# Kernel optimization log

Measured on AMD Instinct MI355X. Metric: run time of the kernel, lower is better.

Reference implementation:

```python
import jax, jax.numpy as jnp
import numpy as np
from jax import lax

B, CIN, H, W = 2, 512, 64, 64
CD = CIN // 2            # down_dim = 256
CQ = CD // 8             # q/k channels = 32
EPS = 1e-5               # BatchNorm eps


def _conv3(x, w, b):
    # 3x3 conv, stride 1, padding 1 (init padding=1), NCHW/OIHW
    y = lax.conv_general_dilated(x, w, (1, 1), [(1, 1), (1, 1)],
                                 dimension_numbers=('NCHW', 'OIHW', 'NCHW'))
    return y + b[None, :, None, None]


def _bn(x, g, b, m, v):
    scale = g / jnp.sqrt(v + EPS)
    return x * scale[None, :, None, None] + (b - m * scale)[None, :, None, None]


def _prelu(x, a):
    return jnp.where(x > 0, x, a * x)


def _p1(x, w, b):
    # 1x1 conv as channel matmul
    return jnp.einsum('bchw,oc->bohw', x, w) + b[None, :, None, None]


def setup_inputs() -> dict:
    key = jax.random.key(0)
    it = iter(jax.random.split(key, 64))
    def nrm(shape, s=0.05):
        return jax.random.normal(next(it), shape, jnp.float32) * s
    inp = {
        'input_rgb': jax.random.normal(next(it), (B, CIN, H, W), jnp.float32),
        'input_dsm': jax.random.normal(next(it), (B, CIN, H, W), jnp.float32),
    }
    for m in ('rgb', 'dsm'):
        inp['conv_w_' + m] = nrm((CD, CIN, 3, 3))
        inp['conv_b_' + m] = nrm((CD,))
        inp['bn_g_' + m] = 1.0 + nrm((CD,))
        inp['bn_b_' + m] = nrm((CD,))
        inp['bn_m_' + m] = nrm((CD,))
        inp['bn_v_' + m] = jax.random.uniform(next(it), (CD,), jnp.float32, 0.5, 1.5)
        inp['prelu_' + m] = jnp.float32(0.25)
        inp['q_w_' + m] = nrm((CQ, CD)); inp['q_b_' + m] = nrm((CQ,))
        inp['k_w_' + m] = nrm((CQ, CD)); inp['k_b_' + m] = nrm((CQ,))
        inp['v_w_' + m] = nrm((CD, CD)); inp['v_b_' + m] = nrm((CD,))
        inp['up_w_' + m] = nrm((CIN, CD)); inp['up_b_' + m] = nrm((CIN,))
        inp['gamma_' + m] = jnp.float32(0.1)  # learned residual gate (zero-init in torch)
    return inp


def reference(input_rgb, input_dsm,
              conv_w_rgb, conv_b_rgb, bn_g_rgb, bn_b_rgb, bn_m_rgb, bn_v_rgb, prelu_rgb,
              q_w_rgb, q_b_rgb, k_w_rgb, k_b_rgb, v_w_rgb, v_b_rgb, up_w_rgb, up_b_rgb, gamma_rgb,
              conv_w_dsm, conv_b_dsm, bn_g_dsm, bn_b_dsm, bn_m_dsm, bn_v_dsm, prelu_dsm,
              q_w_dsm, q_b_dsm, k_w_dsm, k_b_dsm, v_w_dsm, v_b_dsm, up_w_dsm, up_b_dsm, gamma_dsm):
    conv_rgb = _prelu(_bn(_conv3(input_rgb, conv_w_rgb, conv_b_rgb),
                          bn_g_rgb, bn_b_rgb, bn_m_rgb, bn_v_rgb), prelu_rgb)
    conv_dsm = _prelu(_bn(_conv3(input_dsm, conv_w_dsm, conv_b_dsm),
                          bn_g_dsm, bn_b_dsm, bn_m_dsm, bn_v_dsm), prelu_dsm)
    b, c, h, w = conv_rgb.shape
    n = h * w
    q_rgb = _p1(conv_rgb, q_w_rgb, q_b_rgb).reshape(b, CQ, n)
    k_rgb = _p1(conv_rgb, k_w_rgb, k_b_rgb).reshape(b, CQ, n)
    v_rgb = _p1(conv_rgb, v_w_rgb, v_b_rgb).reshape(b, c, n)
    q_dsm = _p1(conv_dsm, q_w_dsm, q_b_dsm).reshape(b, CQ, n)
    k_dsm = _p1(conv_dsm, k_w_dsm, k_b_dsm).reshape(b, CQ, n)
    v_dsm = _p1(conv_dsm, v_w_dsm, v_b_dsm).reshape(b, c, n)
    # cross-modal unscaled attention: dsm queries attend over rgb keys
    attn_rgb = jax.nn.softmax(jnp.einsum('bqn,bqm->bnm', q_dsm, k_rgb), axis=-1)  # [b,n,n]
    o_rgb = jnp.einsum('bcj,bij->bci', v_rgb, attn_rgb).reshape(b, c, h, w)
    o_rgb = gamma_rgb * o_rgb + conv_rgb
    attn_dsm = jax.nn.softmax(jnp.einsum('bqn,bqm->bnm', q_rgb, k_dsm), axis=-1)
    o_dsm = jnp.einsum('bcj,bij->bci', v_dsm, attn_dsm).reshape(b, c, h, w)
    o_dsm = gamma_dsm * o_dsm + conv_dsm
    out_rgb = _p1(o_rgb, up_w_rgb, up_b_rgb) + input_rgb
    out_dsm = _p1(o_dsm, up_w_dsm, up_b_dsm) + input_dsm
    return (out_rgb, out_dsm)
```

## Files before the change

kernel.cpp:

```cpp
#include <hip/hip_runtime.h>
#include <hip/hip_bf16.h>
#include <stdint.h>


constexpr int CINCH = 512;
constexpr int NPIX  = 4096;

typedef __bf16 bf16x8 __attribute__((ext_vector_type(8)));
typedef __bf16 bf16x4 __attribute__((ext_vector_type(4)));
typedef float  f32x4  __attribute__((ext_vector_type(4)));

__device__ __forceinline__ __bf16 f2b(float f) {
    __hip_bfloat16 h = __float2bfloat16(f);
    return *reinterpret_cast<__bf16*>(&h);
}

__device__ __forceinline__ void load_lds16(const void* g, void* l) {
    __builtin_amdgcn_global_load_lds(
        (const __attribute__((address_space(1))) unsigned int*)(uintptr_t)g,
        (__attribute__((address_space(3))) unsigned int*)(uintptr_t)l,
        16, 0, 0);
}

__global__ __launch_bounds__(256)
void prep_w(const float* __restrict__ w_r, const float* __restrict__ w_d,
            const float* __restrict__ cb_r, const float* __restrict__ bg_r,
            const float* __restrict__ bb_r, const float* __restrict__ bm_r,
            const float* __restrict__ bv_r,
            const float* __restrict__ cb_d, const float* __restrict__ bg_d,
            const float* __restrict__ bb_d, const float* __restrict__ bm_d,
            const float* __restrict__ bv_d,
            __bf16* __restrict__ Wt, float* __restrict__ scA,
            float* __restrict__ shB, __bf16* __restrict__ zrow)
{
    const int t = threadIdx.x;
    const int blk = blockIdx.x;
    if (blk < 2304) {
        int gid = blk * 1024 + t * 4;
        int mod = gid >= 1179648;
        int o2  = gid - mod * 1179648;
        int tap = o2 >> 17;
        int r   = o2 & 131071;
        int oc  = r >> 9;
        int ic  = r & 511;
        const float* wsrc = mod ? w_d : w_r;
        long base = ((long)(oc * 512 + ic)) * 9 + tap;
        bf16x4 v;
        v.x = f2b(wsrc[base]);
        v.y = f2b(wsrc[base + 9]);
        v.z = f2b(wsrc[base + 18]);
        v.w = f2b(wsrc[base + 27]);
        *(bf16x4*)&Wt[gid] = v;
    } else if (blk == 2304) {
        unsigned short* z = (unsigned short*)zrow;
        z[t] = 0; z[t + 256] = 0;
    } else {
        int mod = blk - 2305;
        const float* cb = mod ? cb_d : cb_r;
        const float* bg = mod ? bg_d : bg_r;
        const float* bb = mod ? bb_d : bb_r;
        const float* bm = mod ? bm_d : bm_r;
        const float* bv = mod ? bv_d : bv_r;
        int oc = t;
        float sc = bg[oc] * rsqrtf(bv[oc] + 1e-5f);
        scA[mod * 256 + oc] = sc;
        shB[mod * 256 + oc] = (cb[oc] - bm[oc]) * sc + bb[oc];
    }
}

__global__ __launch_bounds__(256)
void prep_gw(const float* __restrict__ qw_r, const float* __restrict__ qw_d,
             const float* __restrict__ kw_r, const float* __restrict__ kw_d,
             const float* __restrict__ vw_r, const float* __restrict__ vw_d,
             const float* __restrict__ uw_r, const float* __restrict__ uw_d,
             __bf16* __restrict__ Wq, __bf16* __restrict__ Wk,
             __bf16* __restrict__ Wv, __bf16* __restrict__ Wu)
{
    int gid = blockIdx.x * 1024 + threadIdx.x * 4;
    __bf16* dst;
    float4 f = make_float4(0.f, 0.f, 0.f, 0.f);
    if (gid < 65536) {
        int mod = gid >> 15, e = gid & 32767;
        dst = Wq + gid;
        if (e < 8192) f = *(const float4*)((mod ? qw_d : qw_r) + e);
    } else if (gid < 131072) {
        int g = gid - 65536;
        int mod = g >> 15, e = g & 32767;
        dst = Wk + g;
        if (e < 8192) f = *(const float4*)((mod ? kw_d : kw_r) + e);
    } else if (gid < 262144) {
        int g = gid - 131072;
        int mod = g >> 16, e = g & 65535;
        dst = Wv + g;
        f = *(const float4*)((mod ? vw_d : vw_r) + e);
    } else {
        int g = gid - 262144;
        int mod = g >> 17, e = g & 131071;
        dst = Wu + g;
        f = *(const float4*)((mod ? uw_d : uw_r) + e);
    }
    bf16x4 o; o.x = f2b(f.x); o.y = f2b(f.y); o.z = f2b(f.z); o.w = f2b(f.w);
    *(bf16x4*)dst = o;
}

__global__ __launch_bounds__(256)
void xpose(const float* __restrict__ inr, const float* __restrict__ ind,
           __bf16* __restrict__ Xp)
{
    __shared__ float tile[32][33];
    const int t = threadIdx.x;
    const int p0 = blockIdx.x * 32;
    const int ic0 = blockIdx.y * 32;
    const int mb = blockIdx.z;
    const int mod = mb >> 1, b = mb & 1;
    const float* src = (mod ? ind : inr) + (long)b * CINCH * NPIX;

    int i = t >> 3, j4 = (t & 7) * 4;
    float4 v = *(const float4*)&src[(long)(ic0 + i) * NPIX + p0 + j4];
    tile[i][j4 + 0] = v.x; tile[i][j4 + 1] = v.y;
    tile[i][j4 + 2] = v.z; tile[i][j4 + 3] = v.w;
    __syncthreads();
    int j = t >> 3, i4 = (t & 7) * 4;
    bf16x4 o;
    o.x = f2b(tile[i4 + 0][j]);
    o.y = f2b(tile[i4 + 1][j]);
    o.z = f2b(tile[i4 + 2][j]);
    o.w = f2b(tile[i4 + 3][j]);
    *(bf16x4*)&Xp[((long)mb * NPIX + p0 + j) * 512 + ic0 + i4] = o;
}

__global__ __launch_bounds__(256)
void t256(const float* __restrict__ src, __bf16* __restrict__ dst)
{
    __shared__ float tile[32][33];
    const int t = threadIdx.x;
    const int p0 = blockIdx.x * 32;
    const int c0 = blockIdx.y * 32;
    const int mb = blockIdx.z;
    const float* s = src + (long)mb * 256 * NPIX;
    __bf16* d = dst + (long)mb * NPIX * 256;

    int i = t >> 3, j4 = (t & 7) * 4;
    float4 v = *(const float4*)&s[(long)(c0 + i) * NPIX + p0 + j4];
    tile[i][j4 + 0] = v.x; tile[i][j4 + 1] = v.y;
    tile[i][j4 + 2] = v.z; tile[i][j4 + 3] = v.w;
    __syncthreads();
    int j = t >> 3, i4 = (t & 7) * 4;
    bf16x4 o;
    o.x = f2b(tile[i4 + 0][j]); o.y = f2b(tile[i4 + 1][j]);
    o.z = f2b(tile[i4 + 2][j]); o.w = f2b(tile[i4 + 3][j]);
    *(bf16x4*)&d[((long)(p0 + j)) * 256 + c0 + i4] = o;
}

__global__ __launch_bounds__(512)
void conv_mfma(const __bf16* __restrict__ Wt, const __bf16* __restrict__ Xp,
               const __bf16* __restrict__ zrow, const float* __restrict__ scA,
               const float* __restrict__ shB, const float* __restrict__ prr,
               const float* __restrict__ prd, float* __restrict__ conv)
{
    __shared__ __bf16 As[3 * 64 * 64];
    __shared__ __bf16 Bs[2 * 385 * 64];

    const int t = threadIdx.x;
    const int y0 = blockIdx.x * 4;
    const int m0 = blockIdx.y * 64;
    const int mb = blockIdx.z;
    const int mod = mb >> 1;

    const __bf16* Am = Wt + (long)mod * (9 * 256 * 512);
    const __bf16* Xb = Xp + (long)mb * NPIX * 512;

    const int lane = t & 63, quad = lane >> 4, l15 = lane & 15, w = t >> 6;
    const int wy = w & 3, wo = w >> 2;

    if (t < 16)
        *(f32x4*)((char*)Bs + (t >> 3) * 49280 + 49152 + (t & 7) * 16) = (f32x4)0.f;
    asm volatile("s_waitcnt lgkmcnt(0)" ::: "memory");

    auto stage_a = [&](int buf, int tap, int cc) {
        int r  = w * 8 + (lane >> 3);
        int sl = (lane & 7) ^ (r & 7);
        const __bf16* src = Am + (long)tap * 131072 + (long)(m0 + r) * 512
                          + cc * 64 + sl * 8;
        load_lds16(src, (char*)As + buf * 8192 + w * 1024);
    };
    auto stage_b = [&](int buf, int cc) {
#pragma unroll
        for (int k = 0; k < 6; ++k) {
            int r  = w * 48 + k * 8 + (lane >> 3);
            int sl = (lane & 7) ^ (r & 7);
            int hr = r >> 6, xx = r & 63;
            int gy = y0 + hr - 1;
            const __bf16* src = ((unsigned)gy < 64u)
                ? Xb + (long)(gy * 64 + xx) * 512 + cc * 64 + sl * 8
                : zrow + sl * 8;
            load_lds16(src, (char*)Bs + buf * 49280 + (w * 48 + k * 8) * 128);
        }
    };

    f32x4 acc[2][4];
#pragma unroll
    for (int i = 0; i < 2; ++i)
#pragma unroll
        for (int j = 0; j < 4; ++j) acc[i][j] = (f32x4)0.f;

    stage_b(0, 0);
    stage_a(0, 0, 0);
    stage_a(1, 1, 0);

    const int soffA0 = ((quad ^ (l15 & 7)) << 4);
    const int soffA1 = (((4 | quad) ^ (l15 & 7)) << 4);

    for (int c = 0; c < 8; ++c) {
        for (int tp = 0; tp < 9; ++tp) {
            const int s = c * 9 + tp;
            if (s == 71)                  { asm volatile("s_waitcnt vmcnt(0)" ::: "memory"); }
            else if (tp >= 7 && c < 7)    { asm volatile("s_waitcnt vmcnt(7)" ::: "memory"); }
            else                          { asm volatile("s_waitcnt vmcnt(1)" ::: "memory"); }
            __builtin_amdgcn_sched_barrier(0);
            __builtin_amdgcn_s_barrier();
            __builtin_amdgcn_sched_barrier(0);

            if (s + 2 < 72) {
                int c2 = (tp + 2 >= 9) ? c + 1 : c;
                int t2 = (tp + 2 >= 9) ? tp - 7 : tp + 2;
                int b2 = (s + 2) % 3;
                stage_a(b2, t2, c2);
            }
            __builtin_amdgcn_sched_barrier(0);
            if (tp == 6 && c < 7) stage_b((c + 1) & 1, c + 1);
            __builtin_amdgcn_sched_barrier(0);

            const char* ab = (const char*)As + (s % 3) * 8192;
            const char* bb = (const char*)Bs + (c & 1) * 49280;
            const int dy = tp / 3 - 1, dx = tp % 3 - 1;
            const int hr = wy + 1 + dy;
            int rb[4];
#pragma unroll
            for (int fj = 0; fj < 4; ++fj) {
                int x = fj * 16 + l15 + dx;
                rb[fj] = ((unsigned)x < 64u) ? hr * 64 + x : 384;
            }
#pragma unroll
            for (int kk = 0; kk < 2; ++kk) {
                const int slq = kk * 4 + quad;
                bf16x8 af[2], bfr[4];
#pragma unroll
                for (int i = 0; i < 2; ++i)
                    af[i] = *(const bf16x8*)(ab + (wo * 32 + 16 * i + l15) * 128
                                             + (kk ? soffA1 : soffA0));
#pragma unroll
                for (int fj = 0; fj < 4; ++fj)
                    bfr[fj] = *(const bf16x8*)(bb + rb[fj] * 128
                                               + ((slq ^ (rb[fj] & 7)) << 4));
#pragma unroll
                for (int i = 0; i < 2; ++i)
#pragma unroll
                    for (int fj = 0; fj < 4; ++fj)
                        acc[i][fj] = __builtin_amdgcn_mfma_f32_16x16x32_bf16(
                            af[i], bfr[fj], acc[i][fj], 0, 0, 0);
            }
        }
    }

    const float alpha = (mod ? prd : prr)[0];
    float* outp = conv + (long)mb * 256 * NPIX;
    const int nbase = (y0 + wy) * 64;
#pragma unroll
    for (int i = 0; i < 2; ++i) {
#pragma unroll
        for (int r = 0; r < 4; ++r) {
            int oc = m0 + wo * 32 + 16 * i + quad * 4 + r;
            float sc = scA[mod * 256 + oc];
            float sh = shB[mod * 256 + oc];
            float* orow = outp + (long)oc * NPIX;
#pragma unroll
            for (int fj = 0; fj < 4; ++fj) {
                int n = nbase + 16 * fj + l15;
                float y = acc[i][fj][r] * sc + sh;
                y = (y > 0.f) ? y : alpha * y;
                orow[n] = y;
            }
        }
    }
}

__global__ __launch_bounds__(256)
void proj_mfma(const __bf16* __restrict__ Wb, int mstride,
               const __bf16* __restrict__ Bt,
               const float* __restrict__ bias_r, const float* __restrict__ bias_d,
               __bf16* __restrict__ dstT, __bf16* __restrict__ dstV,
               float* __restrict__ dstU,
               const float* __restrict__ resid_r, const float* __restrict__ resid_d,
               int mode, float oscale)
{
    __shared__ __bf16 As[128 * 32];
    __shared__ __bf16 Bs[128 * 32];

    const int t = threadIdx.x;
    const int n0 = blockIdx.x * 128;
    const int m0 = blockIdx.y * 128;
    const int mb = blockIdx.z;
    const int mod = mb >> 1, b = mb & 1;

    const __bf16* Am = Wb + (long)mod * mstride;
    const __bf16* Bm = Bt + (long)mb * (NPIX * 256);
    const float* bias = mod ? bias_d : bias_r;

    const int rowa = t >> 2, c16 = t & 3;
    char* ldsA0 = (char*)As + (t >> 6) * 1024;
    char* ldsA1 = ldsA0 + 4096;
    char* ldsB0 = (char*)Bs + (t >> 6) * 1024;
    char* ldsB1 = ldsB0 + 4096;
    const __bf16* srcA = Am + (long)(m0 + rowa) * 256 + c16 * 8;
    const __bf16* srcB = Bm + (long)(n0 + rowa) * 256 + c16 * 8;

    const int lane = t & 63, quad = lane >> 4, l15 = lane & 15, w = t >> 6;
    const int mw = (w >> 1) * 64, nw = (w & 1) * 64;
    const char* abase = (const char*)As + (mw + l15) * 64 + quad * 16;
    const char* bbase = (const char*)Bs + (nw + l15) * 64 + quad * 16;

    f32x4 acc[4][4];
#pragma unroll
    for (int i = 0; i < 4; ++i)
#pragma unroll
        for (int j = 0; j < 4; ++j) acc[i][j] = (f32x4)0.f;

    for (int kc = 0; kc < 256; kc += 32) {
        load_lds16(srcA + kc, ldsA0);
        load_lds16(srcA + kc + 16384, ldsA1);
        load_lds16(srcB + kc, ldsB0);
        load_lds16(srcB + kc + 16384, ldsB1);
        __syncthreads();

        bf16x8 af[4], bfr[4];
#pragma unroll
        for (int i = 0; i < 4; ++i) af[i]  = *(const bf16x8*)(abase + i * 1024);
#pragma unroll
        for (int j = 0; j < 4; ++j) bfr[j] = *(const bf16x8*)(bbase + j * 1024);
#pragma unroll
        for (int i = 0; i < 4; ++i)
#pragma unroll
            for (int j = 0; j < 4; ++j)
                acc[i][j] = __builtin_amdgcn_mfma_f32_16x16x32_bf16(
                    af[i], bfr[j], acc[i][j], 0, 0, 0);
        __syncthreads();
    }

    if (mode == 0) {
        if (mw == 0) {
            __bf16* dbase = dstT + (long)mb * (NPIX * 32);
#pragma unroll
            for (int fi = 0; fi < 2; ++fi)
#pragma unroll
                for (int r = 0; r < 4; ++r) {
                    int oc = 16 * fi + quad * 4 + r;
                    float bi = bias[oc];
#pragma unroll
                    for (int fj = 0; fj < 4; ++fj) {
                        int n = n0 + nw + 16 * fj + l15;
                        dbase[(long)n * 32 + oc] = f2b((acc[fi][fj][r] + bi) * oscale);
                    }
                }
        }
    } else if (mode == 1) {
        __bf16* dv = dstV + (long)mb * (256 * NPIX);
#pragma unroll
        for (int fi = 0; fi < 4; ++fi)
#pragma unroll
            for (int r = 0; r < 4; ++r) {
                int c = m0 + mw + 16 * fi + quad * 4 + r;
                float bi = bias[c];
                __bf16* row = dv + (long)c * NPIX;
#pragma unroll
                for (int fj = 0; fj < 4; ++fj) {
                    int n = n0 + nw + 16 * fj + l15;
                    row[n] = f2b(acc[fi][fj][r] + bi);
                }
            }
    } else {
        float* du = dstU + (long)mod * 4194304 + (long)b * 2097152;
        const float* rs = (mod ? resid_d : resid_r) + (long)b * 2097152;
#pragma unroll
        for (int fi = 0; fi < 4; ++fi)
#pragma unroll
            for (int r = 0; r < 4; ++r) {
                int oc = m0 + mw + 16 * fi + quad * 4 + r;
                float bi = bias[oc];
                const float* rrow = rs + (long)oc * NPIX;
                float* orow = du + (long)oc * NPIX;
#pragma unroll
                for (int fj = 0; fj < 4; ++fj) {
                    int n = n0 + nw + 16 * fj + l15;
                    orow[n] = acc[fi][fj][r] + bi + rrow[n];
                }
            }
    }
}

__global__ __launch_bounds__(256)
void attn_stats_mfma(const __bf16* __restrict__ Qt, const __bf16* __restrict__ Kt,
                     float* __restrict__ rmp, float* __restrict__ rlp)
{
    __shared__ __bf16 Qs[128 * 32];
    __shared__ __bf16 Ks[128 * 32];
    __shared__ float redm[2][128];
    __shared__ float redl[2][128];

    const int t  = threadIdx.x;
    const int i0 = blockIdx.x * 128;
    const int mbo = blockIdx.y;
    const int o  = mbo >> 1, b = mbo & 1;
    const int seg = blockIdx.z;
    const int jbase = seg * 1024;
    const int mbK = o * 2 + b, mbQ = (1 - o) * 2 + b;

    const __bf16* Qg = Qt + (long)mbQ * 131072;
    const __bf16* Kg = Kt + (long)mbK * 131072;

    const int lane = t & 63, quad = lane >> 4, l15 = lane & 15, w = t >> 6;
    const int mS = (w >> 1) * 64;
    const int nS = (w & 1) * 64;

    const int drow = w * 16 + (lane >> 2);
    const int ssl  = ((lane & 3) ^ ((lane >> 3) & 3)) * 16;
    const int rsl  = (quad ^ ((l15 >> 1) & 3)) << 4;

    load_lds16((const char*)Qg + (long)(i0 + drow) * 64 + ssl, (char*)Qs + w * 1024);
    load_lds16((const char*)Qg + (long)(i0 + 64 + drow) * 64 + ssl,
               (char*)Qs + 4096 + w * 1024);
    __syncthreads();

    bf16x8 qa[4];
#pragma unroll
    for (int fi = 0; fi < 4; ++fi)
        qa[fi] = *(const bf16x8*)((const char*)Qs + (mS + 16 * fi + l15) * 64 + rsl);

    const f32x4 zero4 = (f32x4)0.f;
    float m_t[16], l_t[16];
#pragma unroll
    for (int e = 0; e < 16; ++e) { m_t[e] = -3.0e38f; l_t[e] = 0.f; }

    for (int j0 = jbase; j0 < jbase + 1024; j0 += 128) {
        __syncthreads();
        load_lds16((const char*)Kg + (long)(j0 + drow) * 64 + ssl, (char*)Ks + w * 1024);
        load_lds16((const char*)Kg + (long)(j0 + 64 + drow) * 64 + ssl,
                   (char*)Ks + 4096 + w * 1024);
        __syncthreads();

        bf16x8 kb[4];
#pragma unroll
        for (int fj = 0; fj < 4; ++fj)
            kb[fj] = *(const bf16x8*)((const char*)Ks + (nS + 16 * fj + l15) * 64 + rsl);
#pragma unroll
        for (int fi = 0; fi < 4; ++fi) {
            f32x4 sf[4];
#pragma unroll
            for (int fj = 0; fj < 4; ++fj)
                sf[fj] = __builtin_amdgcn_mfma_f32_16x16x32_bf16(qa[fi], kb[fj], zero4, 0, 0, 0);
#pragma unroll
            for (int r = 0; r < 4; ++r) {
                int e = fi * 4 + r;
                float a = fmaxf(fmaxf(sf[0][r], sf[1][r]), fmaxf(sf[2][r], sf[3][r]));
                float nm = fmaxf(m_t[e], a);
                float s = exp2f(sf[0][r] - nm) + exp2f(sf[1][r] - nm)
                        + exp2f(sf[2][r] - nm) + exp2f(sf[3][r] - nm);
                l_t[e] = l_t[e] * exp2f(m_t[e] - nm) + s;
                m_t[e] = nm;
            }
        }
    }

#pragma unroll
    for (int d = 1; d < 16; d <<= 1)
#pragma unroll
        for (int e = 0; e < 16; ++e) {
            float om = __shfl_xor(m_t[e], d, 64);
            float ol = __shfl_xor(l_t[e], d, 64);
            float nm = fmaxf(m_t[e], om);
            l_t[e] = l_t[e] * exp2f(m_t[e] - nm) + ol * exp2f(om - nm);
            m_t[e] = nm;
        }
    if (l15 == 0) {
#pragma unroll
        for (int fi = 0; fi < 4; ++fi)
#pragma unroll
            for (int r = 0; r < 4; ++r) {
                redm[w & 1][mS + 16 * fi + quad * 4 + r] = m_t[fi * 4 + r];
                redl[w & 1][mS + 16 * fi + quad * 4 + r] = l_t[fi * 4 + r];
            }
    }
    __syncthreads();
    if (t < 128) {
        float m0 = redm[0][t], m1 = redm[1][t];
        float l0 = redl[0][t], l1 = redl[1][t];
        float m = fmaxf(m0, m1);
        float l = l0 * exp2f(m0 - m) + l1 * exp2f(m1 - m);
        rmp[seg * 16384 + mbo * 4096 + i0 + t] = m;
        rlp[seg * 16384 + mbo * 4096 + i0 + t] = l;
    }
}

__global__ __launch_bounds__(256)
void stats_merge(const float* __restrict__ rmp, const float* __restrict__ rlp,
                 float* __restrict__ rmb, float* __restrict__ rlb)
{
    int idx = blockIdx.x * 256 + threadIdx.x;
    float m = rmp[idx];
#pragma unroll
    for (int s = 1; s < 4; ++s) m = fmaxf(m, rmp[s * 16384 + idx]);
    float l = 0.f;
#pragma unroll
    for (int s = 0; s < 4; ++s)
        l += rlp[s * 16384 + idx] * exp2f(rmp[s * 16384 + idx] - m);
    rmb[idx] = m;
    rlb[idx] = 1.f / l;
}

__global__ __launch_bounds__(256, 2)
void attn_pv_mfma(const __bf16* __restrict__ Qt, const __bf16* __restrict__ Kt,
                  const __bf16* __restrict__ Vb,
                  float* __restrict__ part0, float* __restrict__ part1,
                  const float* __restrict__ rmb, const float* __restrict__ rlb)
{
    __shared__ __bf16 Qs[64 * 32];
    __shared__ __bf16 Ks[64 * 32];
    __shared__ __bf16 Vs[2 * 256 * 32];
    __shared__ __bf16 Ps[64 * 64];

    const int t  = threadIdx.x;
    const int bx = blockIdx.x;
    const int grp = bx & 7;
    const int i0  = (bx >> 3) * 64;
    const int seg = grp & 1;
    const int mb  = grp >> 1;
    const int o  = mb >> 1, b = mb & 1;
    const int mbQ = (1 - o) * 2 + b;
    const int jbase = seg * 2048;

    const __bf16* Qg = Qt + (long)mbQ * 131072;
    const __bf16* Kg = Kt + (long)mb * 131072;
    const __bf16* Vg = Vb + (long)mb * 1048576;
    const float* rm = rmb + mb * 4096;
    const float* rl = rlb + mb * 4096;

    const int lane = t & 63, quad = lane >> 4, l15 = lane & 15, w = t >> 6;
    const int iS = w * 16;
    const int cw = w * 64;

    const int drow = w * 16 + (lane >> 2);
    const int ssl  = ((lane & 3) ^ ((lane >> 3) & 3)) * 16;
    const int rsl  = (quad ^ ((l15 >> 1) & 3)) << 4;

    load_lds16((const char*)Qg + (long)(i0 + drow) * 64 + ssl, (char*)Qs + w * 1024);

    float mlv[4], rlv[4];
#pragma unroll
    for (int r = 0; r < 4; ++r) mlv[r] = rm[i0 + iS + quad * 4 + r];
#pragma unroll
    for (int fj = 0; fj < 4; ++fj) rlv[fj] = rl[i0 + 16 * fj + l15];

    f32x4 acc[4][4];
#pragma unroll
    for (int i = 0; i < 4; ++i)
#pragma unroll
        for (int j = 0; j < 4; ++j) acc[i][j] = (f32x4)0.f;
    const f32x4 zero4 = (f32x4)0.f;

    __syncthreads();
    const bf16x8 qa = *(const bf16x8*)((const char*)Qs + (iS + l15) * 64 + rsl);

    for (int j0 = jbase; j0 < jbase + 2048; j0 += 64) {
        __syncthreads();
        load_lds16((const char*)Kg + (long)(j0 + drow) * 64 + ssl,
                   (char*)Ks + w * 1024);
        __syncthreads();

#pragma unroll
        for (int ii = 0; ii < 8; ++ii) {
            int ks = ii >> 2;
            int c  = (ii & 3) * 64 + drow;
            load_lds16((const char*)Vg + (long)c * 8192 + (long)(j0 + ks * 32) * 2 + ssl,
                       (char*)Vs + ii * 4096 + w * 1024);
        }

        f32x4 sA[4];
#pragma unroll
        for (int fj = 0; fj < 4; ++fj) {
            bf16x8 kb = *(const bf16x8*)((const char*)Ks + (16 * fj + l15) * 64 + rsl);
            sA[fj] = __builtin_amdgcn_mfma_f32_16x16x32_bf16(qa, kb, zero4, 0, 0, 0);
        }
#pragma unroll
        for (int fj = 0; fj < 4; ++fj)
#pragma unroll
            for (int r = 0; r < 4; ++r) {
                int il = iS + quad * 4 + r;
                int boff = (il * 128 + (16 * fj + l15) * 2) ^ ((il & 7) << 4);
                *(__bf16*)((char*)Ps + boff) = f2b(exp2f(sA[fj][r] - mlv[r]));
            }
        __syncthreads();

#pragma unroll
        for (int ks = 0; ks < 2; ++ks) {
            bf16x8 va[4], pb[4];
#pragma unroll
            for (int fi = 0; fi < 4; ++fi)
                va[fi] = *(const bf16x8*)((const char*)Vs + ks * 16384 +
                                          (cw + 16 * fi + l15) * 64 + rsl);
#pragma unroll
            for (int fj = 0; fj < 4; ++fj) {
                int ip = 16 * fj + l15;
                int boff = (ip * 128 + ks * 64 + quad * 16) ^ ((ip & 7) << 4);
                pb[fj] = *(const bf16x8*)((const char*)Ps + boff);
            }
#pragma unroll
            for (int fi = 0; fi < 4; ++fi)
#pragma unroll
                for (int fj = 0; fj < 4; ++fj)
                    acc[fi][fj] = __builtin_amdgcn_mfma_f32_16x16x32_bf16(
                        va[fi], pb[fj], acc[fi][fj], 0, 0, 0);
        }
    }

    float* pg = (seg ? part1 : part0) + (long)mb * 1048576;
#pragma unroll
    for (int fi = 0; fi < 4; ++fi) {
#pragma unroll
        for (int r = 0; r < 4; ++r) {
            int c = cw + 16 * fi + quad * 4 + r;
            float* zr = pg + (long)c * 4096;
#pragma unroll
            for (int fj = 0; fj < 4; ++fj)
                zr[i0 + 16 * fj + l15] = acc[fi][fj][r] * rlv[fj];
        }
    }
}

__global__ __launch_bounds__(256)
void zred_t(const float* __restrict__ p0, const float* __restrict__ p1,
            const float* __restrict__ convb, __bf16* __restrict__ Zt,
            const float* __restrict__ g_r, const float* __restrict__ g_d)
{
    __shared__ float tile[32][33];
    const int t = threadIdx.x;
    const int pix0 = blockIdx.x * 32;
    const int c0 = blockIdx.y * 32;
    const int mb = blockIdx.z;
    const int o = mb >> 1;
    const float gamma = (o ? g_d : g_r)[0];
    const long base = (long)mb * 1048576;

    int i = t >> 3, j4 = (t & 7) * 4;
    long row = base + (long)(c0 + i) * 4096 + pix0 + j4;
    float4 a = *(const float4*)&p0[row];
    float4 b = *(const float4*)&p1[row];
    float4 cv = *(const float4*)&convb[row];
    tile[i][j4 + 0] = gamma * (a.x + b.x) + cv.x;
    tile[i][j4 + 1] = gamma * (a.y + b.y) + cv.y;
    tile[i][j4 + 2] = gamma * (a.z + b.z) + cv.z;
    tile[i][j4 + 3] = gamma * (a.w + b.w) + cv.w;
    __syncthreads();
    int j = t >> 3, i4 = (t & 7) * 4;
    bf16x4 oq;
    oq.x = f2b(tile[i4 + 0][j]); oq.y = f2b(tile[i4 + 1][j]);
    oq.z = f2b(tile[i4 + 2][j]); oq.w = f2b(tile[i4 + 3][j]);
    *(bf16x4*)&Zt[(long)mb * NPIX * 256 + (long)(pix0 + j) * 256 + c0 + i4] = oq;
}

extern "C" void kernel_launch(void* const* d_in, const int* in_sizes, int n_in,
                              void* d_out, int out_size, void* d_ws, size_t ws_size,
                              hipStream_t stream)
{
    const float* in_rgb = (const float*)d_in[0];
    const float* in_dsm = (const float*)d_in[1];
    auto P = [&](int i) { return (const float*)d_in[i]; };

    float* ws    = (float*)d_ws;
    float* conv  = ws;
    float* part0 = ws + 4194304;
    float* rmb   = ws + 8388608;
    float* rlb   = ws + 8404992;
    float* rmp   = part0;
    float* rlp   = part0 + 65536;
    float* scA   = ws + 8486912;
    float* shB   = ws + 8487424;
    __bf16* zrow = (__bf16*)(ws + 8487936);
    __bf16* Wt   = (__bf16*)(ws + 8488192);
    __bf16* Xp   = (__bf16*)(ws + 9667840);
    float*  part1 = ws + 9667840;
    __bf16* Qt   = (__bf16*)(ws + 13862144);
    __bf16* Kt   = (__bf16*)(ws + 14124288);
    __bf16* Vbb  = (__bf16*)(ws + 14386432);
    __bf16* Ct   = (__bf16*)(ws + 16483584);
    __bf16* Zt   = (__bf16*)(ws + 18580736);
    __bf16* Wq   = (__bf16*)(ws + 20677888);
    __bf16* Wk   = (__bf16*)(ws + 20710656);
    __bf16* Wv   = (__bf16*)(ws + 20743424);
    __bf16* Wu   = (__bf16*)(ws + 20808960);

    prep_w<<<2307, 256, 0, stream>>>(
        P(2), P(18), P(3), P(4), P(5), P(6), P(7),
        P(19), P(20), P(21), P(22), P(23),
        Wt, scA, shB, zrow);
    prep_gw<<<512, 256, 0, stream>>>(
        P(9), P(25), P(11), P(27), P(13), P(29), P(15), P(31),
        Wq, Wk, Wv, Wu);
    xpose<<<dim3(128, 16, 4), 256, 0, stream>>>(in_rgb, in_dsm, Xp);

    conv_mfma<<<dim3(16, 4, 4), 512, 0, stream>>>(
        Wt, Xp, zrow, scA, shB, P(8), P(24), conv);
    t256<<<dim3(128, 8, 4), 256, 0, stream>>>(conv, Ct);

    proj_mfma<<<dim3(32, 1, 4), 256, 0, stream>>>(
        Wq, 32768, Ct, P(10), P(26), Qt, nullptr, nullptr, nullptr, nullptr,
        0, 1.4426950408889634f);
    proj_mfma<<<dim3(32, 1, 4), 256, 0, stream>>>(
        Wk, 32768, Ct, P(12), P(28), Kt, nullptr, nullptr, nullptr, nullptr,
        0, 1.0f);
    proj_mfma<<<dim3(32, 2, 4), 256, 0, stream>>>(
        Wv, 65536, Ct, P(14), P(30), nullptr, Vbb, nullptr, nullptr, nullptr,
        1, 1.0f);

    attn_stats_mfma<<<dim3(32, 4, 4), 256, 0, stream>>>(Qt, Kt, rmp, rlp);
    stats_merge<<<64, 256, 0, stream>>>(rmp, rlp, rmb, rlb);

    attn_pv_mfma<<<512, 256, 0, stream>>>(
        Qt, Kt, Vbb, part0, part1, rmb, rlb);

    zred_t<<<dim3(128, 8, 4), 256, 0, stream>>>(
        part0, part1, conv, Zt, P(17), P(33));

    proj_mfma<<<dim3(32, 4, 4), 256, 0, stream>>>(
        Wu, 131072, Zt, P(16), P(32), nullptr, nullptr, (float*)d_out,
        in_rgb, in_dsm, 2, 1.0f);
}
```

Baseline: 357.0 us.

## Triple-buffer K tiles with prefetch and manual waitcnt barriers in attn_pv

The K tile for the attention PV kernel now goes into a 3-slot LDS ring and is prefetched two iterations ahead. The per-iteration __syncthreads pairs are replaced with raw s_barrier plus explicit vmcnt/lgkmcnt waits, which lets the K prefetch stay in flight while the V loads and MFMAs run. s_setprio is raised around the PV MFMA block. In exchange the kernel uses 8KB more LDS and relies on hand-counted vmcnt values, which is fragile if the number of outstanding loads changes.

```diff
diff --git a/kernel.cpp b/kernel.cpp
--- a/kernel.cpp
+++ b/kernel.cpp
@@ -524,7 +524,7 @@
                   const float* __restrict__ rmb, const float* __restrict__ rlb)
 {
     __shared__ __bf16 Qs[64 * 32];
-    __shared__ __bf16 Ks[64 * 32];
+    __shared__ __bf16 Ks[3 * 64 * 32];
     __shared__ __bf16 Vs[2 * 256 * 32];
     __shared__ __bf16 Ps[64 * 64];
 
@@ -552,13 +552,27 @@
     const int ssl  = ((lane & 3) ^ ((lane >> 3) & 3)) * 16;
     const int rsl  = (quad ^ ((l15 >> 1) & 3)) << 4;
 
+    float mlv[4], rlv[4];
+#pragma unroll
+    for (int r = 0; r < 4; ++r) mlv[r] = rm[i0 + iS + quad * 4 + r];
+#pragma unroll
+    for (int fj = 0; fj < 4; ++fj) rlv[fj] = rl[i0 + 16 * fj + l15];
+    asm volatile("s_waitcnt vmcnt(0)" ::: "memory");
+
+    auto stageK = [&](int s) {
+        const int j0 = jbase + s * 64;
+        load_lds16((const char*)Kg + (long)(j0 + drow) * 64 + ssl,
+                   (char*)Ks + (s % 3) * 4096 + w * 1024);
+    };
+
     load_lds16((const char*)Qg + (long)(i0 + drow) * 64 + ssl, (char*)Qs + w * 1024);
-
-    float mlv[4], rlv[4];
-#pragma unroll
-    for (int r = 0; r < 4; ++r) mlv[r] = rm[i0 + iS + quad * 4 + r];
-#pragma unroll
-    for (int fj = 0; fj < 4; ++fj) rlv[fj] = rl[i0 + 16 * fj + l15];
+    stageK(0);
+    stageK(1);
+    asm volatile("s_waitcnt vmcnt(1)" ::: "memory");
+    __builtin_amdgcn_sched_barrier(0);
+    __builtin_amdgcn_s_barrier();
+    __builtin_amdgcn_sched_barrier(0);
+    const bf16x8 qa = *(const bf16x8*)((const char*)Qs + (iS + l15) * 64 + rsl);
 
     f32x4 acc[4][4];
 #pragma unroll
@@ -567,14 +581,12 @@
         for (int j = 0; j < 4; ++j) acc[i][j] = (f32x4)0.f;
     const f32x4 zero4 = (f32x4)0.f;
 
-    __syncthreads();
-    const bf16x8 qa = *(const bf16x8*)((const char*)Qs + (iS + l15) * 64 + rsl);
-
-    for (int j0 = jbase; j0 < jbase + 2048; j0 += 64) {
-        __syncthreads();
-        load_lds16((const char*)Kg + (long)(j0 + drow) * 64 + ssl,
-                   (char*)Ks + w * 1024);
-        __syncthreads();
+    for (int s = 0; s < 32; ++s) {
+        const int j0 = jbase + s * 64;
+
+        __builtin_amdgcn_sched_barrier(0);
+        __builtin_amdgcn_s_barrier();
+        __builtin_amdgcn_sched_barrier(0);
 
 #pragma unroll
         for (int ii = 0; ii < 8; ++ii) {
@@ -583,11 +595,13 @@
             load_lds16((const char*)Vg + (long)c * 8192 + (long)(j0 + ks * 32) * 2 + ssl,
                        (char*)Vs + ii * 4096 + w * 1024);
         }
-
+        if (s + 2 < 32) stageK(s + 2);
+
+        const char* kbp = (const char*)Ks + (s % 3) * 4096;
         f32x4 sA[4];
 #pragma unroll
         for (int fj = 0; fj < 4; ++fj) {
-            bf16x8 kb = *(const bf16x8*)((const char*)Ks + (16 * fj + l15) * 64 + rsl);
+            bf16x8 kb = *(const bf16x8*)(kbp + (16 * fj + l15) * 64 + rsl);
             sA[fj] = __builtin_amdgcn_mfma_f32_16x16x32_bf16(qa, kb, zero4, 0, 0, 0);
         }
 #pragma unroll
@@ -598,8 +612,14 @@
                 int boff = (il * 128 + (16 * fj + l15) * 2) ^ ((il & 7) << 4);
                 *(__bf16*)((char*)Ps + boff) = f2b(exp2f(sA[fj][r] - mlv[r]));
             }
-        __syncthreads();
-
+
+        if (s < 30) { asm volatile("s_waitcnt vmcnt(1) lgkmcnt(0)" ::: "memory"); }
+        else        { asm volatile("s_waitcnt vmcnt(0) lgkmcnt(0)" ::: "memory"); }
+        __builtin_amdgcn_sched_barrier(0);
+        __builtin_amdgcn_s_barrier();
+        __builtin_amdgcn_sched_barrier(0);
+
+        __builtin_amdgcn_s_setprio(1);
 #pragma unroll
         for (int ks = 0; ks < 2; ++ks) {
             bf16x8 va[4], pb[4];
@@ -620,6 +640,7 @@
                     acc[fi][fj] = __builtin_amdgcn_mfma_f32_16x16x32_bf16(
                         va[fi], pb[fj], acc[fi][fj], 0, 0, 0);
         }
+        __builtin_amdgcn_s_setprio(0);
     }
 
     float* pg = (seg ? part1 : part0) + (long)mb * 1048576;
```

Result: no change. 359.5 us (+0.7%).
